# Kernel tuning notes

Measured on AMD Instinct MI355X. Metric: run time of the kernel, lower is better.

The kernel has to match this reference:

```python
import jax, jax.numpy as jnp
import numpy as np
import math

B, T, D, H, L = 8, 1024, 128, 8, 2
DH = D // H            # head dim = 16
F = 2 * D              # ffn hidden = 256 (FFN_EXPANSION=2)
SCALE = math.sqrt(DH)  # sqrt of Q last dim per head


def layernorm(x, g, b):
    m = jnp.mean(x, axis=-1, keepdims=True)
    v = jnp.var(x, axis=-1, keepdims=True)
    return (x - m) * jax.lax.rsqrt(v + 1e-5) * g + b


def setup_inputs() -> dict:
    key = jax.random.key(0)
    ks = jax.random.split(key, 16)
    s = 1.0 / math.sqrt(D)
    r = lambda i, shp: jax.random.normal(ks[i], shp, dtype=jnp.float32) * s
    return {
        "x": jax.random.normal(ks[0], (B, T, D), dtype=jnp.float32),
        "y": jax.random.normal(ks[1], (B, T, D), dtype=jnp.float32),
        # shared qkv projections (no bias), per layer
        "Wq": r(2, (L, D, D)), "Wk": r(3, (L, D, D)), "Wv": r(4, (L, D, D)),
        "Wox": r(5, (L, D, D)), "box": jnp.zeros((L, D), jnp.float32),
        "Woy": r(6, (L, D, D)), "boy": jnp.zeros((L, D), jnp.float32),
        "ln1x_g": jnp.ones((L, D), jnp.float32), "ln1x_b": jnp.zeros((L, D), jnp.float32),
        "ln1y_g": jnp.ones((L, D), jnp.float32), "ln1y_b": jnp.zeros((L, D), jnp.float32),
        "ln2x_g": jnp.ones((L, D), jnp.float32), "ln2x_b": jnp.zeros((L, D), jnp.float32),
        "ln2y_g": jnp.ones((L, D), jnp.float32), "ln2y_b": jnp.zeros((L, D), jnp.float32),
        "fx_w1": r(7, (L, D, F)), "fx_b1": jnp.zeros((L, F), jnp.float32),
        "fx_w2": r(8, (L, F, D)), "fx_b2": jnp.zeros((L, D), jnp.float32),
        "fy_w1": r(9, (L, D, F)), "fy_b1": jnp.zeros((L, F), jnp.float32),
        "fy_w2": r(10, (L, F, D)), "fy_b2": jnp.zeros((L, D), jnp.float32),
    }


def _heads(t):
    # (B,T,D) -> (B,T,H,DH)
    return t.reshape(B, T, H, DH)


def _block(x, y, Wq, Wk, Wv, Wox, box, Woy, boy,
           ln1x_g, ln1x_b, ln1y_g, ln1y_b, ln2x_g, ln2x_b, ln2y_g, ln2y_b,
           fx_w1, fx_b1, fx_w2, fx_b2, fy_w1, fy_b1, fy_w2, fy_b2):
    xn = layernorm(x, ln1x_g, ln1x_b)
    yn = layernorm(y, ln1y_g, ln1y_b)
    # x-branch: Q from y, K/V from x ; y-branch: Q from x, K/V from y
    qx = _heads(yn @ Wq); kx = _heads(xn @ Wk); vx = _heads(xn @ Wv)
    qy = _heads(xn @ Wq); ky = _heads(yn @ Wk); vy = _heads(yn @ Wv)
    ax = jnp.einsum('bthd,bshd->bhts', qx, kx)  # (B,H,T,T)
    ay = jnp.einsum('bthd,bshd->bhts', qy, ky)
    # cat over heads + reshape(B,2,H,T,T) + mean(dim=1) == per-head average
    w = jax.nn.softmax((ax + ay) * (0.5 / SCALE), axis=-1)
    o1 = jnp.einsum('bhts,bshd->bthd', w, vx).reshape(B, T, D) @ Wox + box
    o2 = jnp.einsum('bhts,bshd->bthd', w, vy).reshape(B, T, D) @ Woy + boy
    x = x + o1
    y = y + o2
    xn2 = layernorm(x, ln2x_g, ln2x_b)
    yn2 = layernorm(y, ln2y_g, ln2y_b)
    x = x + jax.nn.gelu(xn2 @ fx_w1 + fx_b1, approximate=False) @ fx_w2 + fx_b2
    y = y + jax.nn.gelu(yn2 @ fy_w1 + fy_b1, approximate=False) @ fy_w2 + fy_b2
    return x, y


def reference(x, y, Wq, Wk, Wv, Wox, box, Woy, boy,
              ln1x_g, ln1x_b, ln1y_g, ln1y_b, ln2x_g, ln2x_b, ln2y_g, ln2y_b,
              fx_w1, fx_b1, fx_w2, fx_b2, fy_w1, fy_b1, fy_w2, fy_b2):
    for i in range(L):
        x, y = _block(x, y, Wq[i], Wk[i], Wv[i], Wox[i], box[i], Woy[i], boy[i],
                      ln1x_g[i], ln1x_b[i], ln1y_g[i], ln1y_b[i],
                      ln2x_g[i], ln2x_b[i], ln2y_g[i], ln2y_b[i],
                      fx_w1[i], fx_b1[i], fx_w2[i], fx_b2[i],
                      fy_w1[i], fy_b1[i], fy_w2[i], fy_b2[i])
    return (x, y)
```

## Files before the change

kernel.cpp:

```cpp
#include <hip/hip_runtime.h>
#include <cstddef>

#define BB   8
#define TT   1024
#define DDIM 128
#define HH   8
#define DHH  16
#define FF   256
#define BT   (BB * TT)

typedef unsigned short u16;
typedef __attribute__((ext_vector_type(8))) short short8;
typedef __attribute__((ext_vector_type(4))) float f32x4;

__device__ __forceinline__ u16 bf(float x) {
  unsigned u = __builtin_bit_cast(unsigned, x);
  u += 0x7fffu + ((u >> 16) & 1u);
  return (u16)(u >> 16);
}
__device__ __forceinline__ u16 bft(float x) {
  return (u16)(__builtin_bit_cast(unsigned, x) >> 16);
}

__device__ __forceinline__ float gelu_f(float x) {
  const float t = x * (0.79788456f + 0.03567740814f * x * x);
  return x / (1.0f + __expf(-2.0f * t));
}

struct PrepP { const float* W; u16* Wt; int K; int N; };
struct PrepArgs { PrepP p[18]; };

__global__ __launch_bounds__(256) void prep_k(PrepArgs a) {
  const PrepP pp = a.p[blockIdx.z];
  const int n0 = blockIdx.x * 64, k0 = blockIdx.y * 64;
  if (n0 >= pp.N || k0 >= pp.K) return;
  __shared__ float tile[64][65];
  const int tid = threadIdx.x;
  #pragma unroll
  for (int t = tid; t < 1024; t += 256) {
    const int kk = t >> 4, nn4 = (t & 15) << 2;
    float4 v = *(const float4*)(pp.W + (size_t)(k0 + kk) * pp.N + n0 + nn4);
    tile[nn4 + 0][kk] = v.x; tile[nn4 + 1][kk] = v.y;
    tile[nn4 + 2][kk] = v.z; tile[nn4 + 3][kk] = v.w;
  }
  __syncthreads();
  #pragma unroll
  for (int t = tid; t < 1024; t += 256) {
    const int nn = t >> 4, kk4 = (t & 15) << 2;
    ushort4 o;
    o.x = bf(tile[nn][kk4 + 0]); o.y = bf(tile[nn][kk4 + 1]);
    o.z = bf(tile[nn][kk4 + 2]); o.w = bf(tile[nn][kk4 + 3]);
    *(ushort4*)(pp.Wt + (size_t)(n0 + nn) * pp.K + k0 + kk4) = o;
  }
}

__global__ __launch_bounds__(256) void ln0_k(const float* __restrict__ X,
                                             const float* __restrict__ Y,
                                             const float* __restrict__ gx,
                                             const float* __restrict__ bx,
                                             const float* __restrict__ gy,
                                             const float* __restrict__ by,
                                             u16* __restrict__ ox,
                                             u16* __restrict__ oy) {
  const int which = blockIdx.y;
  const float* in = which ? Y : X;
  const float* g  = which ? gy : gx;
  const float* b  = which ? by : bx;
  u16* out        = which ? oy : ox;
  const int row  = blockIdx.x * 4 + (threadIdx.x >> 6);
  const int lane = threadIdx.x & 63;

  float2 v = *(const float2*)(in + (size_t)row * DDIM + lane * 2);
  float s  = v.x + v.y;
  float sq = v.x * v.x + v.y * v.y;
  #pragma unroll
  for (int off = 32; off >= 1; off >>= 1) {
    s  += __shfl_xor(s, off);
    sq += __shfl_xor(sq, off);
  }
  const float mean = s * (1.0f / DDIM);
  const float var  = sq * (1.0f / DDIM) - mean * mean;
  const float r    = rsqrtf(var + 1e-5f);
  float2 gg = *(const float2*)(g + lane * 2);
  float2 bb = *(const float2*)(b + lane * 2);
  ushort2 o;
  o.x = bf((v.x - mean) * r * gg.x + bb.x);
  o.y = bf((v.y - mean) * r * gg.y + bb.y);
  *(ushort2*)(out + (size_t)row * DDIM + lane * 2) = o;
}

struct GemmP { const u16* A; const u16* Wt; const float* bias; const float* res;
               float* outF; u16* outB; const float* g; const float* b; };
struct GemmArgs { GemmP p[6]; int K; int N; int gelu; int ln; };

__global__ __launch_bounds__(256) void gemmf_k(GemmArgs a) {
  const GemmP pp = a.p[blockIdx.z];
  const int K = a.K, N = a.N;
  const int n0 = blockIdx.x * 128, m0 = blockIdx.y * 32;
  __shared__ __align__(16) u16 As[32][72];
  __shared__ __align__(16) u16 Bs[128][72];
  __shared__ float2 stats[32][2];
  const int tid  = threadIdx.x;
  const int w    = tid >> 6;
  const int lane = tid & 63;
  const int l15  = lane & 15;
  const int quad = lane >> 4;
  const int wr = w & 1, wc = w >> 1;

  f32x4 acc[4];
  #pragma unroll
  for (int j = 0; j < 4; ++j) acc[j] = {0.f, 0.f, 0.f, 0.f};

  for (int k0 = 0; k0 < K; k0 += 64) {
    {
      const int row = tid >> 3, c8 = (tid & 7) << 3;
      *(short8*)&As[row][c8] = *(const short8*)(pp.A + (size_t)(m0 + row) * K + k0 + c8);
    }
    #pragma unroll
    for (int t = tid; t < 1024; t += 256) {
      const int row = t >> 3, c8 = (t & 7) << 3;
      *(short8*)&Bs[row][c8] = *(const short8*)(pp.Wt + (size_t)(n0 + row) * K + k0 + c8);
    }
    __syncthreads();
    #pragma unroll
    for (int ks = 0; ks < 2; ++ks) {
      short8 ar = *(const short8*)&As[wr * 16 + l15][ks * 32 + quad * 8];
      #pragma unroll
      for (int j = 0; j < 4; ++j) {
        short8 br = *(const short8*)&Bs[wc * 64 + j * 16 + l15][ks * 32 + quad * 8];
        acc[j] = __builtin_amdgcn_mfma_f32_16x16x32_bf16(ar, br, acc[j], 0, 0, 0);
      }
    }
    __syncthreads();
  }

  #pragma unroll
  for (int j = 0; j < 4; ++j) {
    const int n = n0 + wc * 64 + j * 16 + l15;
    const float bias_v = pp.bias ? pp.bias[n] : 0.f;
    #pragma unroll
    for (int reg = 0; reg < 4; ++reg) {
      const int m = m0 + wr * 16 + quad * 4 + reg;
      float v = acc[j][reg] + bias_v;
      if (a.gelu) v = gelu_f(v);
      if (pp.res) v += pp.res[(size_t)m * N + n];
      acc[j][reg] = v;
      if (pp.outF) pp.outF[(size_t)m * N + n] = v;
    }
  }

  if (!a.ln) {
    if (pp.outB) {
      #pragma unroll
      for (int j = 0; j < 4; ++j) {
        const int n = n0 + wc * 64 + j * 16 + l15;
        #pragma unroll
        for (int reg = 0; reg < 4; ++reg) {
          const int m = m0 + wr * 16 + quad * 4 + reg;
          pp.outB[(size_t)m * N + n] = bf(acc[j][reg]);
        }
      }
    }
    return;
  }

  #pragma unroll
  for (int reg = 0; reg < 4; ++reg) {
    float s = 0.f, q = 0.f;
    #pragma unroll
    for (int j = 0; j < 4; ++j) { const float v = acc[j][reg]; s += v; q += v * v; }
    #pragma unroll
    for (int off = 8; off >= 1; off >>= 1) {
      s += __shfl_xor(s, off, 16);
      q += __shfl_xor(q, off, 16);
    }
    if (l15 == 0) stats[wr * 16 + quad * 4 + reg][wc] = make_float2(s, q);
  }
  __syncthreads();
  #pragma unroll
  for (int reg = 0; reg < 4; ++reg) {
    const int mloc = wr * 16 + quad * 4 + reg;
    const float2 s0 = stats[mloc][0], s1 = stats[mloc][1];
    const float mean = (s0.x + s1.x) * (1.0f / 128.f);
    const float var  = (s0.y + s1.y) * (1.0f / 128.f) - mean * mean;
    const float r    = rsqrtf(var + 1e-5f);
    #pragma unroll
    for (int j = 0; j < 4; ++j) {
      const int n = wc * 64 + j * 16 + l15;
      pp.outB[(size_t)(m0 + mloc) * 128 + n] =
          bf((acc[j][reg] - mean) * r * pp.g[n] + pp.b[n]);
    }
  }
}

__global__ __launch_bounds__(256) void attn_k(const u16* __restrict__ qx,
                                              const u16* __restrict__ kx,
                                              const u16* __restrict__ vx,
                                              const u16* __restrict__ qy,
                                              const u16* __restrict__ ky,
                                              const u16* __restrict__ vy,
                                              u16* __restrict__ o1,
                                              u16* __restrict__ o2) {
  const int t0 = blockIdx.x * 64;
  const int bh = blockIdx.y;
  const int b = bh >> 3, h = bh & 7;
  const size_t base = (size_t)b * TT * DDIM + h * DHH;

  __shared__ __align__(16) u16 Ks[2][64][40];
  __shared__ __align__(16) u16 Vt[2][32][72];
  __shared__ __align__(16) u16 Ps[64][72];

  const int tid  = threadIdx.x;
  const int w    = tid >> 6;
  const int lane = tid & 63;
  const int l15  = lane & 15;
  const int quad = lane >> 4;

  const u16* qp = (quad < 2) ? qx : qy;
  const int dq = (quad & 1) * 8;
  const short8 qa = *(const short8*)(qp + base + (size_t)(t0 + w * 16 + l15) * DDIM + dq);

  f32x4 Of0 = {0.f, 0.f, 0.f, 0.f};
  f32x4 Of1 = {0.f, 0.f, 0.f, 0.f};
  float l_i[4] = {0.f, 0.f, 0.f, 0.f};

  const int ks_s = tid >> 2, ks_c = tid & 3;
  const u16* ks_p = (ks_c < 2) ? kx : ky;
  const int ks_d8 = (ks_c & 1) * 8;
  const int ks_col = (ks_c < 2 ? 0 : 16) + ks_d8;

  #define STAGE(kt, buf)                                                          \
    do {                                                                          \
      const int s0_ = (kt) * 64;                                                  \
      *(short8*)&Ks[buf][ks_s][ks_col] =                                          \
          *(const short8*)(ks_p + base + (size_t)(s0_ + ks_s) * DDIM + ks_d8);    \
      _Pragma("unroll")                                                           \
      for (int t = tid; t < 512; t += 256) {                                      \
        const int c = t & 31;                                                     \
        const int sb = (t >> 5) << 2;                                             \
        const u16* vp = (c < 16) ? vx : vy;                                       \
        const int cc = c & 15;                                                    \
        const size_t ro = base + (size_t)(s0_ + sb) * DDIM + cc;                  \
        ushort4 w4;                                                               \
        w4.x = vp[ro];                                                            \
        w4.y = vp[ro + DDIM];                                                     \
        w4.z = vp[ro + 2 * DDIM];                                                 \
        w4.w = vp[ro + 3 * DDIM];                                                 \
        *(ushort4*)&Vt[buf][c][sb] = w4;                                          \
      }                                                                           \
    } while (0)

  STAGE(0, 0);

  for (int kt = 0; kt < TT / 64; ++kt) {
    const int buf = kt & 1;
    __syncthreads();
    if (kt + 1 < TT / 64) STAGE(kt + 1, buf ^ 1);

    f32x4 Sf[4];
    #pragma unroll
    for (int t = 0; t < 4; ++t) {
      short8 kb = *(const short8*)&Ks[buf][t * 16 + l15][quad * 8];
      f32x4 z = {0.f, 0.f, 0.f, 0.f};
      Sf[t] = __builtin_amdgcn_mfma_f32_16x16x32_bf16(qa, kb, z, 0, 0, 0);
    }

    #pragma unroll
    for (int reg = 0; reg < 4; ++reg) {
      const float p0 = exp2f(Sf[0][reg] * 0.18033688011112042f);
      const float p1 = exp2f(Sf[1][reg] * 0.18033688011112042f);
      const float p2 = exp2f(Sf[2][reg] * 0.18033688011112042f);
      const float p3 = exp2f(Sf[3][reg] * 0.18033688011112042f);
      l_i[reg] += p0 + p1 + p2 + p3;
      const int q = w * 16 + quad * 4 + reg;
      Ps[q][l15]      = bft(p0);
      Ps[q][16 + l15] = bft(p1);
      Ps[q][32 + l15] = bft(p2);
      Ps[q][48 + l15] = bft(p3);
    }

    #pragma unroll
    for (int sh = 0; sh < 2; ++sh) {
      short8 pa  = *(const short8*)&Ps[w * 16 + l15][sh * 32 + quad * 8];
      short8 vb0 = *(const short8*)&Vt[buf][l15][sh * 32 + quad * 8];
      short8 vb1 = *(const short8*)&Vt[buf][16 + l15][sh * 32 + quad * 8];
      Of0 = __builtin_amdgcn_mfma_f32_16x16x32_bf16(pa, vb0, Of0, 0, 0, 0);
      Of1 = __builtin_amdgcn_mfma_f32_16x16x32_bf16(pa, vb1, Of1, 0, 0, 0);
    }
  }
  #undef STAGE

  #pragma unroll
  for (int reg = 0; reg < 4; ++reg) {
    float l = l_i[reg];
    #pragma unroll
    for (int off = 8; off >= 1; off >>= 1) l += __shfl_xor(l, off, 16);
    const float inv = 1.0f / l;
    const size_t r = base + (size_t)(t0 + w * 16 + quad * 4 + reg) * DDIM + l15;
    o1[r] = bf(Of0[reg] * inv);
    o2[r] = bf(Of1[reg] * inv);
  }
}

extern "C" void kernel_launch(void* const* d_in, const int* in_sizes, int n_in,
                              void* d_out, int out_size, void* d_ws, size_t ws_size,
                              hipStream_t stream) {
  const float* x_in  = (const float*)d_in[0];
  const float* y_in  = (const float*)d_in[1];
  const float* Wq    = (const float*)d_in[2];
  const float* Wk    = (const float*)d_in[3];
  const float* Wv    = (const float*)d_in[4];
  const float* Wox   = (const float*)d_in[5];
  const float* box   = (const float*)d_in[6];
  const float* Woy   = (const float*)d_in[7];
  const float* boy   = (const float*)d_in[8];
  const float* ln1xg = (const float*)d_in[9];
  const float* ln1xb = (const float*)d_in[10];
  const float* ln1yg = (const float*)d_in[11];
  const float* ln1yb = (const float*)d_in[12];
  const float* ln2xg = (const float*)d_in[13];
  const float* ln2xb = (const float*)d_in[14];
  const float* ln2yg = (const float*)d_in[15];
  const float* ln2yb = (const float*)d_in[16];
  const float* fxw1  = (const float*)d_in[17];
  const float* fxb1  = (const float*)d_in[18];
  const float* fxw2  = (const float*)d_in[19];
  const float* fxb2  = (const float*)d_in[20];
  const float* fyw1  = (const float*)d_in[21];
  const float* fyb1  = (const float*)d_in[22];
  const float* fyw2  = (const float*)d_in[23];
  const float* fyb2  = (const float*)d_in[24];

  const size_t S = (size_t)BT * DDIM;
  float* X = (float*)d_out;
  float* Y = X + S;

  char* wsb = (char*)d_ws;
  auto carve = [&](size_t bytes) { char* p = wsb; wsb += (bytes + 255) & ~(size_t)255; return p; };
  u16* xn  = (u16*)carve(S * 2);
  u16* yn  = (u16*)carve(S * 2);
  u16* qx  = (u16*)carve(S * 2);
  u16* kx  = (u16*)carve(S * 2);
  u16* vx  = (u16*)carve(S * 2);
  u16* qy  = (u16*)carve(S * 2);
  u16* ky  = (u16*)carve(S * 2);
  u16* vy  = (u16*)carve(S * 2);
  u16* ob1 = (u16*)carve(S * 2);
  u16* ob2 = (u16*)carve(S * 2);
  u16* hx  = (u16*)carve(2 * S * 2);
  u16* hy  = (u16*)carve(2 * S * 2);
  u16* WqT[2], *WkT[2], *WvT[2], *WoxT[2], *WoyT[2];
  u16* f1xT[2], *f1yT[2], *f2xT[2], *f2yT[2];
  for (int l = 0; l < 2; ++l) {
    WqT[l]  = (u16*)carve(16384 * 2);
    WkT[l]  = (u16*)carve(16384 * 2);
    WvT[l]  = (u16*)carve(16384 * 2);
    WoxT[l] = (u16*)carve(16384 * 2);
    WoyT[l] = (u16*)carve(16384 * 2);
    f1xT[l] = (u16*)carve(32768 * 2);
    f1yT[l] = (u16*)carve(32768 * 2);
    f2xT[l] = (u16*)carve(32768 * 2);
    f2yT[l] = (u16*)carve(32768 * 2);
  }

  {
    PrepArgs a;
    int idx = 0;
    for (int l = 0; l < 2; ++l) {
      a.p[idx++] = {Wq  + (size_t)l * 16384, WqT[l],  128, 128};
      a.p[idx++] = {Wk  + (size_t)l * 16384, WkT[l],  128, 128};
      a.p[idx++] = {Wv  + (size_t)l * 16384, WvT[l],  128, 128};
      a.p[idx++] = {Wox + (size_t)l * 16384, WoxT[l], 128, 128};
      a.p[idx++] = {Woy + (size_t)l * 16384, WoyT[l], 128, 128};
      a.p[idx++] = {fxw1 + (size_t)l * 32768, f1xT[l], 128, 256};
      a.p[idx++] = {fyw1 + (size_t)l * 32768, f1yT[l], 128, 256};
      a.p[idx++] = {fxw2 + (size_t)l * 32768, f2xT[l], 256, 128};
      a.p[idx++] = {fyw2 + (size_t)l * 32768, f2yT[l], 256, 128};
    }
    prep_k<<<dim3(4, 4, 18), 256, 0, stream>>>(a);
  }

  ln0_k<<<dim3(BT / 4, 2), 256, 0, stream>>>(x_in, y_in, ln1xg, ln1xb, ln1yg, ln1yb, xn, yn);

  for (int l = 0; l < 2; ++l) {
    const size_t bo  = (size_t)l * DDIM;
    const size_t fbo = (size_t)l * FF;

    {
      GemmArgs a = {}; a.K = DDIM; a.N = DDIM; a.gelu = 0; a.ln = 0;
      a.p[0] = {yn, WqT[l], nullptr, nullptr, nullptr, qx, nullptr, nullptr};
      a.p[1] = {xn, WkT[l], nullptr, nullptr, nullptr, kx, nullptr, nullptr};
      a.p[2] = {xn, WvT[l], nullptr, nullptr, nullptr, vx, nullptr, nullptr};
      a.p[3] = {xn, WqT[l], nullptr, nullptr, nullptr, qy, nullptr, nullptr};
      a.p[4] = {yn, WkT[l], nullptr, nullptr, nullptr, ky, nullptr, nullptr};
      a.p[5] = {yn, WvT[l], nullptr, nullptr, nullptr, vy, nullptr, nullptr};
      gemmf_k<<<dim3(1, BT / 32, 6), 256, 0, stream>>>(a);
    }
    attn_k<<<dim3(TT / 64, BB * HH), 256, 0, stream>>>(qx, kx, vx, qy, ky, vy, ob1, ob2);
    {
      const float* resx = (l == 0) ? x_in : X;
      const float* resy = (l == 0) ? y_in : Y;
      GemmArgs a = {}; a.K = DDIM; a.N = DDIM; a.gelu = 0; a.ln = 1;
      a.p[0] = {ob1, WoxT[l], box + bo, resx, X, xn, ln2xg + bo, ln2xb + bo};
      a.p[1] = {ob2, WoyT[l], boy + bo, resy, Y, yn, ln2yg + bo, ln2yb + bo};
      gemmf_k<<<dim3(1, BT / 32, 2), 256, 0, stream>>>(a);
    }
    {
      GemmArgs a = {}; a.K = DDIM; a.N = FF; a.gelu = 1; a.ln = 0;
      a.p[0] = {xn, f1xT[l], fxb1 + fbo, nullptr, nullptr, hx, nullptr, nullptr};
      a.p[1] = {yn, f1yT[l], fyb1 + fbo, nullptr, nullptr, hy, nullptr, nullptr};
      gemmf_k<<<dim3(2, BT / 32, 2), 256, 0, stream>>>(a);
    }
    {
      GemmArgs a = {}; a.K = FF; a.N = DDIM; a.gelu = 0; a.ln = (l == 0) ? 1 : 0;
      if (l == 0) {
        a.p[0] = {hx, f2xT[l], fxb2 + bo, X, X, xn, ln1xg + DDIM, ln1xb + DDIM};
        a.p[1] = {hy, f2yT[l], fyb2 + bo, Y, Y, yn, ln1yg + DDIM, ln1yb + DDIM};
      } else {
        a.p[0] = {hx, f2xT[l], fxb2 + bo, X, X, nullptr, nullptr, nullptr};
        a.p[1] = {hy, f2yT[l], fyb2 + bo, Y, Y, nullptr, nullptr, nullptr};
      }
      gemmf_k<<<dim3(1, BT / 32, 2), 256, 0, stream>>>(a);
    }
  }
}
```

Baseline: 271.7 us.

## Use single-wave register-direct GEMM and load attention K fragments from global

The GEMM kernel becomes a single 64-thread wave that computes a 16x128 tile. It loads A and B fragments straight from global memory into registers for MFMA and drops the LDS staging, the barriers and the cross-wave layernorm stats exchange. The attention kernel likewise loads K fragments directly from global into registers each tile and drops the K shared-memory buffer, keeping LDS only for V and P. This removes LDS round-trips and syncs, but each wave now re-reads weights from global/L2 and gets less coalescing and reuse across waves.

```diff
diff --git a/kernel.cpp b/kernel.cpp
--- a/kernel.cpp
+++ b/kernel.cpp
@@ -93,58 +93,44 @@
                float* outF; u16* outB; const float* g; const float* b; };
 struct GemmArgs { GemmP p[6]; int K; int N; int gelu; int ln; };
 
-__global__ __launch_bounds__(256) void gemmf_k(GemmArgs a) {
+__global__ __launch_bounds__(64) void gemml_k(GemmArgs a) {
   const GemmP pp = a.p[blockIdx.z];
   const int K = a.K, N = a.N;
-  const int n0 = blockIdx.x * 128, m0 = blockIdx.y * 32;
-  __shared__ __align__(16) u16 As[32][72];
-  __shared__ __align__(16) u16 Bs[128][72];
-  __shared__ float2 stats[32][2];
-  const int tid  = threadIdx.x;
-  const int w    = tid >> 6;
-  const int lane = tid & 63;
-  const int l15  = lane & 15;
-  const int quad = lane >> 4;
-  const int wr = w & 1, wc = w >> 1;
-
-  f32x4 acc[4];
-  #pragma unroll
-  for (int j = 0; j < 4; ++j) acc[j] = {0.f, 0.f, 0.f, 0.f};
-
-  for (int k0 = 0; k0 < K; k0 += 64) {
-    {
-      const int row = tid >> 3, c8 = (tid & 7) << 3;
-      *(short8*)&As[row][c8] = *(const short8*)(pp.A + (size_t)(m0 + row) * K + k0 + c8);
-    }
-    #pragma unroll
-    for (int t = tid; t < 1024; t += 256) {
-      const int row = t >> 3, c8 = (t & 7) << 3;
-      *(short8*)&Bs[row][c8] = *(const short8*)(pp.Wt + (size_t)(n0 + row) * K + k0 + c8);
-    }
-    __syncthreads();
-    #pragma unroll
-    for (int ks = 0; ks < 2; ++ks) {
-      short8 ar = *(const short8*)&As[wr * 16 + l15][ks * 32 + quad * 8];
-      #pragma unroll
-      for (int j = 0; j < 4; ++j) {
-        short8 br = *(const short8*)&Bs[wc * 64 + j * 16 + l15][ks * 32 + quad * 8];
-        acc[j] = __builtin_amdgcn_mfma_f32_16x16x32_bf16(ar, br, acc[j], 0, 0, 0);
-      }
-    }
-    __syncthreads();
-  }
-
-  #pragma unroll
-  for (int j = 0; j < 4; ++j) {
-    const int n = n0 + wc * 64 + j * 16 + l15;
+  const int n0 = blockIdx.x * 128;
+  const int m0 = blockIdx.y * 16;
+  const int lane = threadIdx.x;
+  const int l15 = lane & 15, quad = lane >> 4;
+
+  f32x4 acc[8];
+  #pragma unroll
+  for (int j = 0; j < 8; ++j) acc[j] = {0.f, 0.f, 0.f, 0.f};
+
+  const u16* Ap = pp.A  + (size_t)(m0 + l15) * K + quad * 8;
+  const u16* Bp = pp.Wt + (size_t)(n0 + l15) * K + quad * 8;
+  const size_t bstep = (size_t)16 * K;
+
+  #pragma unroll 2
+  for (int k = 0; k < K; k += 32) {
+    const short8 av = *(const short8*)(Ap + k);
+    #pragma unroll
+    for (int j = 0; j < 8; ++j) {
+      const short8 bv = *(const short8*)(Bp + (size_t)j * bstep + k);
+      acc[j] = __builtin_amdgcn_mfma_f32_16x16x32_bf16(av, bv, acc[j], 0, 0, 0);
+    }
+  }
+
+  float vv[8][4];
+  #pragma unroll
+  for (int j = 0; j < 8; ++j) {
+    const int n = n0 + j * 16 + l15;
     const float bias_v = pp.bias ? pp.bias[n] : 0.f;
     #pragma unroll
     for (int reg = 0; reg < 4; ++reg) {
-      const int m = m0 + wr * 16 + quad * 4 + reg;
+      const int m = m0 + quad * 4 + reg;
       float v = acc[j][reg] + bias_v;
       if (a.gelu) v = gelu_f(v);
       if (pp.res) v += pp.res[(size_t)m * N + n];
-      acc[j][reg] = v;
+      vv[j][reg] = v;
       if (pp.outF) pp.outF[(size_t)m * N + n] = v;
     }
   }
@@ -152,13 +138,11 @@
   if (!a.ln) {
     if (pp.outB) {
       #pragma unroll
-      for (int j = 0; j < 4; ++j) {
-        const int n = n0 + wc * 64 + j * 16 + l15;
+      for (int j = 0; j < 8; ++j) {
+        const int n = n0 + j * 16 + l15;
         #pragma unroll
-        for (int reg = 0; reg < 4; ++reg) {
-          const int m = m0 + wr * 16 + quad * 4 + reg;
-          pp.outB[(size_t)m * N + n] = bf(acc[j][reg]);
-        }
+        for (int reg = 0; reg < 4; ++reg)
+          pp.outB[(size_t)(m0 + quad * 4 + reg) * N + n] = bf(vv[j][reg]);
       }
     }
     return;
@@ -168,27 +152,20 @@
   for (int reg = 0; reg < 4; ++reg) {
     float s = 0.f, q = 0.f;
     #pragma unroll
-    for (int j = 0; j < 4; ++j) { const float v = acc[j][reg]; s += v; q += v * v; }
+    for (int j = 0; j < 8; ++j) { const float v = vv[j][reg]; s += v; q += v * v; }
     #pragma unroll
     for (int off = 8; off >= 1; off >>= 1) {
       s += __shfl_xor(s, off, 16);
       q += __shfl_xor(q, off, 16);
     }
-    if (l15 == 0) stats[wr * 16 + quad * 4 + reg][wc] = make_float2(s, q);
-  }
-  __syncthreads();
-  #pragma unroll
-  for (int reg = 0; reg < 4; ++reg) {
-    const int mloc = wr * 16 + quad * 4 + reg;
-    const float2 s0 = stats[mloc][0], s1 = stats[mloc][1];
-    const float mean = (s0.x + s1.x) * (1.0f / 128.f);
-    const float var  = (s0.y + s1.y) * (1.0f / 128.f) - mean * mean;
+    const float mean = s * (1.0f / 128.f);
+    const float var  = q * (1.0f / 128.f) - mean * mean;
     const float r    = rsqrtf(var + 1e-5f);
-    #pragma unroll
-    for (int j = 0; j < 4; ++j) {
-      const int n = wc * 64 + j * 16 + l15;
-      pp.outB[(size_t)(m0 + mloc) * 128 + n] =
-          bf((acc[j][reg] - mean) * r * pp.g[n] + pp.b[n]);
+    const int m = m0 + quad * 4 + reg;
+    #pragma unroll
+    for (int j = 0; j < 8; ++j) {
+      const int n = j * 16 + l15;
+      pp.outB[(size_t)m * 128 + n] = bf((vv[j][reg] - mean) * r * pp.g[n] + pp.b[n]);
     }
   }
 }
@@ -206,7 +183,6 @@
   const int b = bh >> 3, h = bh & 7;
   const size_t base = (size_t)b * TT * DDIM + h * DHH;
 
-  __shared__ __align__(16) u16 Ks[2][64][40];
   __shared__ __align__(16) u16 Vt[2][32][72];
   __shared__ __align__(16) u16 Ps[64][72];
 
@@ -217,23 +193,18 @@
   const int quad = lane >> 4;
 
   const u16* qp = (quad < 2) ? qx : qy;
+  const u16* kp = (quad < 2) ? kx : ky;
   const int dq = (quad & 1) * 8;
   const short8 qa = *(const short8*)(qp + base + (size_t)(t0 + w * 16 + l15) * DDIM + dq);
+  const u16* kfrag = kp + base + (size_t)l15 * DDIM + dq;
 
   f32x4 Of0 = {0.f, 0.f, 0.f, 0.f};
   f32x4 Of1 = {0.f, 0.f, 0.f, 0.f};
   float l_i[4] = {0.f, 0.f, 0.f, 0.f};
 
-  const int ks_s = tid >> 2, ks_c = tid & 3;
-  const u16* ks_p = (ks_c < 2) ? kx : ky;
-  const int ks_d8 = (ks_c & 1) * 8;
-  const int ks_col = (ks_c < 2 ? 0 : 16) + ks_d8;
-
-  #define STAGE(kt, buf)                                                          \
+  #define STAGE_V(kt, buf)                                                        \
     do {                                                                          \
       const int s0_ = (kt) * 64;                                                  \
-      *(short8*)&Ks[buf][ks_s][ks_col] =                                          \
-          *(const short8*)(ks_p + base + (size_t)(s0_ + ks_s) * DDIM + ks_d8);    \
       _Pragma("unroll")                                                           \
       for (int t = tid; t < 512; t += 256) {                                      \
         const int c = t & 31;                                                     \
@@ -250,19 +221,24 @@
       }                                                                           \
     } while (0)
 
-  STAGE(0, 0);
+  STAGE_V(0, 0);
 
   for (int kt = 0; kt < TT / 64; ++kt) {
     const int buf = kt & 1;
+
+    short8 kb[4];
+    #pragma unroll
+    for (int t = 0; t < 4; ++t)
+      kb[t] = *(const short8*)(kfrag + (size_t)(kt * 64 + t * 16) * DDIM);
+
     __syncthreads();
-    if (kt + 1 < TT / 64) STAGE(kt + 1, buf ^ 1);
+    if (kt + 1 < TT / 64) STAGE_V(kt + 1, buf ^ 1);
 
     f32x4 Sf[4];
     #pragma unroll
     for (int t = 0; t < 4; ++t) {
-      short8 kb = *(const short8*)&Ks[buf][t * 16 + l15][quad * 8];
       f32x4 z = {0.f, 0.f, 0.f, 0.f};
-      Sf[t] = __builtin_amdgcn_mfma_f32_16x16x32_bf16(qa, kb, z, 0, 0, 0);
+      Sf[t] = __builtin_amdgcn_mfma_f32_16x16x32_bf16(qa, kb[t], z, 0, 0, 0);
     }
 
     #pragma unroll
@@ -288,7 +264,7 @@
       Of1 = __builtin_amdgcn_mfma_f32_16x16x32_bf16(pa, vb1, Of1, 0, 0, 0);
     }
   }
-  #undef STAGE
+  #undef STAGE_V
 
   #pragma unroll
   for (int reg = 0; reg < 4; ++reg) {
@@ -394,7 +370,7 @@
       a.p[3] = {xn, WqT[l], nullptr, nullptr, nullptr, qy, nullptr, nullptr};
       a.p[4] = {yn, WkT[l], nullptr, nullptr, nullptr, ky, nullptr, nullptr};
       a.p[5] = {yn, WvT[l], nullptr, nullptr, nullptr, vy, nullptr, nullptr};
-      gemmf_k<<<dim3(1, BT / 32, 6), 256, 0, stream>>>(a);
+      gemml_k<<<dim3(1, BT / 16, 6), 64, 0, stream>>>(a);
     }
     attn_k<<<dim3(TT / 64, BB * HH), 256, 0, stream>>>(qx, kx, vx, qy, ky, vy, ob1, ob2);
     {
@@ -403,13 +379,13 @@
       GemmArgs a = {}; a.K = DDIM; a.N = DDIM; a.gelu = 0; a.ln = 1;
       a.p[0] = {ob1, WoxT[l], box + bo, resx, X, xn, ln2xg + bo, ln2xb + bo};
       a.p[1] = {ob2, WoyT[l], boy + bo, resy, Y, yn, ln2yg + bo, ln2yb + bo};
-      gemmf_k<<<dim3(1, BT / 32, 2), 256, 0, stream>>>(a);
+      gemml_k<<<dim3(1, BT / 16, 2), 64, 0, stream>>>(a);
     }
     {
       GemmArgs a = {}; a.K = DDIM; a.N = FF; a.gelu = 1; a.ln = 0;
       a.p[0] = {xn, f1xT[l], fxb1 + fbo, nullptr, nullptr, hx, nullptr, nullptr};
       a.p[1] = {yn, f1yT[l], fyb1 + fbo, nullptr, nullptr, hy, nullptr, nullptr};
-      gemmf_k<<<dim3(2, BT / 32, 2), 256, 0, stream>>>(a);
+      gemml_k<<<dim3(2, BT / 16, 2), 64, 0, stream>>>(a);
     }
     {
       GemmArgs a = {}; a.K = FF; a.N = DDIM; a.gelu = 0; a.ln = (l == 0) ? 1 : 0;
@@ -420,7 +396,7 @@
         a.p[0] = {hx, f2xT[l], fxb2 + bo, X, X, nullptr, nullptr, nullptr};
         a.p[1] = {hy, f2yT[l], fyb2 + bo, Y, Y, nullptr, nullptr, nullptr};
       }
-      gemmf_k<<<dim3(1, BT / 32, 2), 256, 0, stream>>>(a);
-    }
-  }
-}
+      gemml_k<<<dim3(1, BT / 16, 2), 64, 0, stream>>>(a);
+    }
+  }
+}
```

Result: slower. 362.4 us (+33.4%).
